# Optimization experiments

Hardware: AMD Instinct MI355X
Metric: run time of the kernel (lower is better)

Reference implementation:

```python
import jax, jax.numpy as jnp
import numpy as np

N_NODES = 100000
N_EDGES = 1600000
D = 128


def sage_conv(x, src, dst, W_l, W_r, b):
    # mean aggregation of source-node features at destination nodes
    msgs = x[src]  # [E, D] gather
    agg = jax.ops.segment_sum(msgs, dst, num_segments=N_NODES)  # [N, D]
    deg = jax.ops.segment_sum(jnp.ones((src.shape[0],), x.dtype), dst,
                              num_segments=N_NODES)
    agg = agg / jnp.maximum(deg, 1.0)[:, None]
    # PyG SAGEConv: lin_l(agg) + lin_r(x) (bias lives in lin_l)
    return agg @ W_l + x @ W_r + b


def setup_inputs() -> dict:
    key = jax.random.key(0)
    ks = jax.random.split(key, 8)
    s = 1.0 / np.sqrt(D)
    x = jax.random.normal(ks[0], (N_NODES, D), dtype=jnp.float32)
    edge_index = jax.random.randint(ks[1], (2, N_EDGES), 0, N_NODES, dtype=jnp.int64)
    W_l1 = jax.random.normal(ks[2], (D, D), dtype=jnp.float32) * s
    W_r1 = jax.random.normal(ks[3], (D, D), dtype=jnp.float32) * s
    b1 = jnp.zeros((D,), dtype=jnp.float32)
    W_l2 = jax.random.normal(ks[4], (D, D), dtype=jnp.float32) * s
    W_r2 = jax.random.normal(ks[5], (D, D), dtype=jnp.float32) * s
    b2 = jnp.zeros((D,), dtype=jnp.float32)
    return {"x": x, "edge_index": edge_index, "W_l1": W_l1, "W_r1": W_r1,
            "b1": b1, "W_l2": W_l2, "W_r2": W_r2, "b2": b2}


def reference(x, edge_index, W_l1, W_r1, b1, W_l2, W_r2, b2):
    src, dst = edge_index[0], edge_index[1]
    h = jax.nn.relu(sage_conv(x, src, dst, W_l1, W_r1, b1))
    h = jax.nn.relu(sage_conv(h, src, dst, W_l2, W_r2, b2))
    return h
```

## Files before the change

kernel.cpp:

```cpp
#include <hip/hip_runtime.h>
#include <hip/hip_bf16.h>
#include <stdint.h>

#define D 128
#define BCAP 18432
typedef unsigned short u16;
typedef unsigned int u32;
typedef __attribute__((ext_vector_type(8))) short bf16x8;
typedef __attribute__((ext_vector_type(4))) float f32x4;
typedef __attribute__((ext_vector_type(2))) float f32x2;
typedef __attribute__((ext_vector_type(2))) unsigned int u32x2;

__device__ inline float bf16lo_to_f(u32 v) {
    u32 u = v << 16; return __builtin_bit_cast(float, u);
}
__device__ inline float bf16hi_to_f(u32 v) {
    u32 u = v & 0xFFFF0000u; return __builtin_bit_cast(float, u);
}
__device__ inline u16 f_to_bf16(float f) {
    u32 u = __builtin_bit_cast(u32, f);
    u += 0x7FFFu + ((u >> 16) & 1u);
    return (u16)(u >> 16);
}
__device__ inline u32 pack_bf16(float a, float b) {
    return (u32)f_to_bf16(a) | ((u32)f_to_bf16(b) << 16);
}

__global__ void zero_ints(int* __restrict__ p, int n) {
    int i = blockIdx.x * blockDim.x + threadIdx.x;
    if (i < n) p[i] = 0;
}

__global__ __launch_bounds__(256) void prep_fused(
    const int* __restrict__ src, const int* __restrict__ dst, int E, int nbuck, int binB,
    uint2* __restrict__ pairs, int* __restrict__ bcur,
    const float* __restrict__ x, u16* __restrict__ xb, int nf4, int convB,
    const float* __restrict__ Wl1, const float* __restrict__ Wr1,
    const float* __restrict__ Wl2, const float* __restrict__ Wr2,
    u16* __restrict__ WT1, u16* __restrict__ WT2) {
    __shared__ int hist[128], gb[128], loc[128];
    int tid = threadIdx.x;
    int bid = blockIdx.x;
    if (bid < binB) {
        if (tid < 128) { hist[tid] = 0; loc[tid] = 0; }
        __syncthreads();
        int base = bid * 4096;
        int d[16], b[16];
        #pragma unroll
        for (int i = 0; i < 16; ++i) {
            int e = base + i * 256 + tid;
            d[i] = (e < E) ? dst[e] : -1;
            b[i] = (d[i] >= 0) ? (d[i] >> 10) : -1;
            if (b[i] >= 0) atomicAdd(&hist[b[i]], 1);
        }
        __syncthreads();
        if (tid < nbuck && hist[tid] > 0) gb[tid] = atomicAdd(&bcur[tid], hist[tid]);
        __syncthreads();
        #pragma unroll
        for (int i = 0; i < 16; ++i) {
            if (b[i] >= 0) {
                int e = base + i * 256 + tid;
                int s = src[e];
                int r = atomicAdd(&loc[b[i]], 1);
                int pos = gb[b[i]] + r;
                if (pos < BCAP)
                    pairs[(size_t)b[i] * BCAP + pos] = make_uint2((u32)s, (u32)d[i]);
            }
        }
    } else if (bid < binB + convB) {
        int idx = (bid - binB) * 256 + tid;
        int stride = convB * 256;
        const float4* xf = (const float4*)x;
        uint2* xo = (uint2*)xb;
        for (int i = idx; i < nf4; i += stride) {
            float4 v = xf[i];
            xo[i] = make_uint2(pack_bf16(v.x, v.y), pack_bf16(v.z, v.w));
        }
    } else {
        int id = (bid - binB - convB) * 256 + tid;
        if (id < 2 * 128 * 256) {
            int which = id >> 15;
            int rem = id & 32767;
            int n = rem >> 8;
            int k = rem & 255;
            const float* Wl = which ? Wl2 : Wl1;
            const float* Wr = which ? Wr2 : Wr1;
            float v = (k < 128) ? Wl[k * 128 + n] : Wr[(k - 128) * 128 + n];
            u16* WT = which ? WT2 : WT1;
            WT[n * 256 + k] = f_to_bf16(v);
        }
    }
}

__global__ __launch_bounds__(256) void build_csr(
    const uint2* __restrict__ pairs, const int* __restrict__ bcur, int N,
    int* __restrict__ cnt, int* __restrict__ seg_start, int* __restrict__ gtotal,
    int* __restrict__ csr_src) {
    __shared__ int cnt_l[1024];
    __shared__ int off_l[1024];
    __shared__ int sblk[256];
    __shared__ int gbase_s;
    int tid = threadIdx.x;
    int bk = blockIdx.x;
    int n0 = bk << 10;
    int nN = min(1024, N - n0);
    #pragma unroll
    for (int i = 0; i < 4; ++i) cnt_l[tid * 4 + i] = 0;
    __syncthreads();
    int m = min(bcur[bk], BCAP);
    const uint2* P = pairs + (size_t)bk * BCAP;
    for (int i = tid; i < m; i += 256) {
        uint2 p = P[i];
        atomicAdd(&cnt_l[(int)p.y - n0], 1);
    }
    __syncthreads();
    int c0 = cnt_l[tid * 4], c1 = cnt_l[tid * 4 + 1], c2 = cnt_l[tid * 4 + 2], c3 = cnt_l[tid * 4 + 3];
    int mysum = c0 + c1 + c2 + c3;
    sblk[tid] = mysum;
    for (int off = 1; off < 256; off <<= 1) {
        __syncthreads();
        int u = (tid >= off) ? sblk[tid - off] : 0;
        __syncthreads();
        sblk[tid] += u;
    }
    int excl = sblk[tid] - mysum;
    off_l[tid * 4]     = excl;
    off_l[tid * 4 + 1] = excl + c0;
    off_l[tid * 4 + 2] = excl + c0 + c1;
    off_l[tid * 4 + 3] = excl + c0 + c1 + c2;
    if (tid == 255) gbase_s = atomicAdd(gtotal, sblk[255]);
    __syncthreads();
    int gbase = gbase_s;
    #pragma unroll
    for (int i = 0; i < 4; ++i) {
        int j = tid * 4 + i;
        if (j < nN) {
            cnt[n0 + j] = cnt_l[j];
            seg_start[n0 + j] = gbase + off_l[j];
        }
    }
    __syncthreads();
    #pragma unroll
    for (int i = 0; i < 4; ++i) cnt_l[tid * 4 + i] = 0;
    __syncthreads();
    for (int i = tid; i < m; i += 256) {
        uint2 p = P[i];
        int dl = (int)p.y - n0;
        int r = atomicAdd(&cnt_l[dl], 1);
        csr_src[gbase + off_l[dl] + r] = (int)p.x;
    }
}

__global__ __launch_bounds__(256) void aggregate_bf16(
    const u16* __restrict__ xb, const int* __restrict__ csr_src,
    const int* __restrict__ seg_start, const int* __restrict__ cnt,
    int N, u16* __restrict__ agg) {
    int wave = threadIdx.x >> 6;
    int lane = threadIdx.x & 63;
    int n = blockIdx.x * (blockDim.x >> 6) + wave;
    if (n >= N) return;
    int s0 = seg_start[n];
    int deg = cnt[n];
    int sub = lane & 15;
    int eoff = lane >> 4;

    f32x2 acc2[4];
    #pragma unroll
    for (int i = 0; i < 4; ++i) acc2[i] = (f32x2){0.f, 0.f};

    for (int c0 = 0; c0 < deg; c0 += 64) {
        int chunkN = min(deg - c0, 64);
        int myidx = (lane < chunkN) ? csr_src[s0 + c0 + lane] : 0;
        for (int e0 = 0; e0 < chunkN; e0 += 16) {
            uint4 v[4];
            bool act[4];
            #pragma unroll
            for (int j = 0; j < 4; ++j) {
                int ej = e0 + j * 4 + eoff;
                act[j] = (ej < chunkN);
                if (e0 + j * 4 < chunkN) {
                    int es = act[j] ? ej : (chunkN - 1);
                    int s = __shfl(myidx, es & 63);
                    v[j] = ((const uint4*)(xb + (size_t)s * 128))[sub];
                }
            }
            #pragma unroll
            for (int j = 0; j < 4; ++j) {
                if (act[j]) {
                    u32 w;
                    w = v[j].x; acc2[0] += __builtin_bit_cast(f32x2, (u32x2){w << 16, w & 0xFFFF0000u});
                    w = v[j].y; acc2[1] += __builtin_bit_cast(f32x2, (u32x2){w << 16, w & 0xFFFF0000u});
                    w = v[j].z; acc2[2] += __builtin_bit_cast(f32x2, (u32x2){w << 16, w & 0xFFFF0000u});
                    w = v[j].w; acc2[3] += __builtin_bit_cast(f32x2, (u32x2){w << 16, w & 0xFFFF0000u});
                }
            }
        }
    }

    float a[8];
    #pragma unroll
    for (int i = 0; i < 4; ++i) { a[2 * i] = acc2[i].x; a[2 * i + 1] = acc2[i].y; }
    #pragma unroll
    for (int i = 0; i < 8; ++i) {
        a[i] += __shfl_xor(a[i], 16);
        a[i] += __shfl_xor(a[i], 32);
    }

    if (eoff == 0) {
        float inv = 1.0f / fmaxf((float)deg, 1.0f);
        uint4 o;
        o.x = pack_bf16(a[0] * inv, a[1] * inv);
        o.y = pack_bf16(a[2] * inv, a[3] * inv);
        o.z = pack_bf16(a[4] * inv, a[5] * inv);
        o.w = pack_bf16(a[6] * inv, a[7] * inv);
        ((uint4*)(agg + (size_t)n * 128))[sub] = o;
    }
}

template<int OUT_BF16>
__global__ __launch_bounds__(256) void sage_gemm(
    const u16* __restrict__ Aa, const u16* __restrict__ Ax,
    const u16* __restrict__ WT, const float* __restrict__ bias,
    void* __restrict__ out, int N) {
    __shared__ u16 Bl[128 * 256];
    int tid = threadIdx.x;

    {
        const uint4* Wg = (const uint4*)WT;
        uint4* Bl4 = (uint4*)Bl;
        #pragma unroll
        for (int i = 0; i < 16; ++i) {
            int cid = tid + 256 * i;
            int n = cid >> 5;
            int kc = cid & 31;
            Bl4[(n << 5) | (kc ^ (n & 15))] = Wg[cid];
        }
    }
    __syncthreads();

    int wavein = tid >> 6;
    int lane = tid & 63;
    int col = lane & 15;
    int chunk = lane >> 4;
    int wid = blockIdx.x * 4 + wavein;

    size_t m0 = (size_t)wid * 32 + col;
    size_t m1 = m0 + 16;
    size_t m0c = (m0 < (size_t)N) ? m0 : (size_t)(N - 1);
    size_t m1c = (m1 < (size_t)N) ? m1 : (size_t)(N - 1);

    const bf16x8* a0p = (const bf16x8*)(Aa + m0c * 128 + chunk * 8);
    const bf16x8* a1p = (const bf16x8*)(Aa + m1c * 128 + chunk * 8);
    const bf16x8* x0p = (const bf16x8*)(Ax + m0c * 128 + chunk * 8);
    const bf16x8* x1p = (const bf16x8*)(Ax + m1c * 128 + chunk * 8);

    f32x4 acc0[8], acc1[8];
    #pragma unroll
    for (int t = 0; t < 8; ++t) {
        acc0[t] = (f32x4){0.f, 0.f, 0.f, 0.f};
        acc1[t] = (f32x4){0.f, 0.f, 0.f, 0.f};
    }

    #pragma unroll
    for (int s = 0; s < 4; ++s) {
        bf16x8 a0 = a0p[s * 4];
        bf16x8 a1 = a1p[s * 4];
        int kc = s * 4 + chunk;
        #pragma unroll
        for (int t = 0; t < 8; ++t) {
            const bf16x8* bp = (const bf16x8*)(Bl + (((16 * t + col) << 8) | ((kc ^ col) << 3)));
            bf16x8 b = *bp;
            acc0[t] = __builtin_amdgcn_mfma_f32_16x16x32_bf16(a0, b, acc0[t], 0, 0, 0);
            acc1[t] = __builtin_amdgcn_mfma_f32_16x16x32_bf16(a1, b, acc1[t], 0, 0, 0);
        }
    }
    #pragma unroll
    for (int s = 0; s < 4; ++s) {
        bf16x8 a0 = x0p[s * 4];
        bf16x8 a1 = x1p[s * 4];
        int kc = 16 + s * 4 + chunk;
        #pragma unroll
        for (int t = 0; t < 8; ++t) {
            const bf16x8* bp = (const bf16x8*)(Bl + (((16 * t + col) << 8) | ((kc ^ col) << 3)));
            bf16x8 b = *bp;
            acc0[t] = __builtin_amdgcn_mfma_f32_16x16x32_bf16(a0, b, acc0[t], 0, 0, 0);
            acc1[t] = __builtin_amdgcn_mfma_f32_16x16x32_bf16(a1, b, acc1[t], 0, 0, 0);
        }
    }

    #pragma unroll
    for (int mt = 0; mt < 2; ++mt) {
        size_t row0 = (size_t)wid * 32 + mt * 16 + chunk * 4;
        #pragma unroll
        for (int t = 0; t < 8; ++t) {
            int n = 16 * t + col;
            float bv = bias[n];
            f32x4 a = mt ? acc1[t] : acc0[t];
            #pragma unroll
            for (int r = 0; r < 4; ++r) {
                size_t row = row0 + r;
                if (row < (size_t)N) {
                    float v = fmaxf(a[r] + bv, 0.f);
                    if (OUT_BF16) ((u16*)out)[row * 128 + n] = f_to_bf16(v);
                    else          ((float*)out)[row * 128 + n] = v;
                }
            }
        }
    }
}

extern "C" void kernel_launch(void* const* d_in, const int* in_sizes, int n_in,
                              void* d_out, int out_size, void* d_ws, size_t ws_size,
                              hipStream_t stream) {
    const float* x   = (const float*)d_in[0];
    const int*   ei  = (const int*)d_in[1];
    const float* Wl1 = (const float*)d_in[2];
    const float* Wr1 = (const float*)d_in[3];
    const float* b1  = (const float*)d_in[4];
    const float* Wl2 = (const float*)d_in[5];
    const float* Wr2 = (const float*)d_in[6];
    const float* b2  = (const float*)d_in[7];
    float* out       = (float*)d_out;

    int N = in_sizes[0] / D;
    int E = in_sizes[1] / 2;
    const int* src = ei;
    const int* dst = ei + E;
    int nbuck = (N + 1023) >> 10;

    char* ws = (char*)d_ws;
    int* cnt       = (int*)ws;  ws += (size_t)N * 4;
    int* seg_start = (int*)ws;  ws += (size_t)N * 4;
    int* bcur      = (int*)ws;  ws += 128 * 4;
    int* gtotal    = (int*)ws;  ws += 4 * 4;
    ws = (char*)(((uintptr_t)ws + 255) & ~(uintptr_t)255);
    int* csr_src   = (int*)ws;  ws += (size_t)E * 4;
    ws = (char*)(((uintptr_t)ws + 255) & ~(uintptr_t)255);
    u16* WT1       = (u16*)ws;  ws += (size_t)128 * 256 * 2;
    u16* WT2       = (u16*)ws;  ws += (size_t)128 * 256 * 2;
    ws = (char*)(((uintptr_t)ws + 255) & ~(uintptr_t)255);
    u16* aggb      = (u16*)ws;  ws += (size_t)N * 128 * 2;
    ws = (char*)(((uintptr_t)ws + 255) & ~(uintptr_t)255);
    u16* h1b       = (u16*)ws;  ws += (size_t)N * 128 * 2;
    u16* xb        = (u16*)d_out;
    uint2* pairs   = (uint2*)aggb;

    zero_ints<<<1, 256, 0, stream>>>(bcur, 132);

    int binB  = (E + 4095) / 4096;
    int convB = 2048;
    int nf4   = N * (D / 4);
    prep_fused<<<binB + convB + 256, 256, 0, stream>>>(
        src, dst, E, nbuck, binB, pairs, bcur,
        x, xb, nf4, convB, Wl1, Wr1, Wl2, Wr2, WT1, WT2);

    build_csr<<<nbuck, 256, 0, stream>>>(pairs, bcur, N, cnt, seg_start, gtotal, csr_src);

    int aggBlocks = (N + 3) / 4;
    int gemmBlocks = (N + 127) / 128;

    aggregate_bf16<<<aggBlocks, 256, 0, stream>>>(xb, csr_src, seg_start, cnt, N, aggb);
    sage_gemm<1><<<gemmBlocks, 256, 0, stream>>>(aggb, xb, WT1, b1, h1b, N);

    aggregate_bf16<<<aggBlocks, 256, 0, stream>>>(h1b, csr_src, seg_start, cnt, N, aggb);
    sage_gemm<0><<<gemmBlocks, 256, 0, stream>>>(aggb, h1b, WT2, b2, out, N);
}
```

Before: 344.8 us.

## Pad bucket counters, widen build_csr to 1024 threads, skip inactive gather loads

Bucket cursors are spaced 32 ints apart so blocks doing atomics on different buckets no longer contend on the same cache line. build_csr now runs 1024 threads per block, one per node slot, which simplifies the scan and doubles pair-scan parallelism but lengthens the scan to 10 barrier-separated steps. The aggregate kernel no longer issues redundant loads for inactive tail edges; instead it predicates the load. These are small, mostly independent tweaks to the preprocessing and gather stages.

```diff
diff --git a/kernel.cpp b/kernel.cpp
--- a/kernel.cpp
+++ b/kernel.cpp
@@ -4,6 +4,7 @@
 
 #define D 128
 #define BCAP 18432
+#define CPAD 32
 typedef unsigned short u16;
 typedef unsigned int u32;
 typedef __attribute__((ext_vector_type(8))) short bf16x8;
@@ -11,12 +12,6 @@
 typedef __attribute__((ext_vector_type(2))) float f32x2;
 typedef __attribute__((ext_vector_type(2))) unsigned int u32x2;
 
-__device__ inline float bf16lo_to_f(u32 v) {
-    u32 u = v << 16; return __builtin_bit_cast(float, u);
-}
-__device__ inline float bf16hi_to_f(u32 v) {
-    u32 u = v & 0xFFFF0000u; return __builtin_bit_cast(float, u);
-}
 __device__ inline u16 f_to_bf16(float f) {
     u32 u = __builtin_bit_cast(u32, f);
     u += 0x7FFFu + ((u >> 16) & 1u);
@@ -54,7 +49,7 @@
             if (b[i] >= 0) atomicAdd(&hist[b[i]], 1);
         }
         __syncthreads();
-        if (tid < nbuck && hist[tid] > 0) gb[tid] = atomicAdd(&bcur[tid], hist[tid]);
+        if (tid < nbuck && hist[tid] > 0) gb[tid] = atomicAdd(&bcur[tid * CPAD], hist[tid]);
         __syncthreads();
         #pragma unroll
         for (int i = 0; i < 16; ++i) {
@@ -92,58 +87,47 @@
     }
 }
 
-__global__ __launch_bounds__(256) void build_csr(
+__global__ __launch_bounds__(1024) void build_csr(
     const uint2* __restrict__ pairs, const int* __restrict__ bcur, int N,
     int* __restrict__ cnt, int* __restrict__ seg_start, int* __restrict__ gtotal,
     int* __restrict__ csr_src) {
     __shared__ int cnt_l[1024];
     __shared__ int off_l[1024];
-    __shared__ int sblk[256];
+    __shared__ int sblk[1024];
     __shared__ int gbase_s;
     int tid = threadIdx.x;
     int bk = blockIdx.x;
     int n0 = bk << 10;
     int nN = min(1024, N - n0);
-    #pragma unroll
-    for (int i = 0; i < 4; ++i) cnt_l[tid * 4 + i] = 0;
-    __syncthreads();
-    int m = min(bcur[bk], BCAP);
+    cnt_l[tid] = 0;
+    __syncthreads();
+    int m = min(bcur[bk * CPAD], BCAP);
     const uint2* P = pairs + (size_t)bk * BCAP;
-    for (int i = tid; i < m; i += 256) {
+    for (int i = tid; i < m; i += 1024) {
         uint2 p = P[i];
         atomicAdd(&cnt_l[(int)p.y - n0], 1);
     }
     __syncthreads();
-    int c0 = cnt_l[tid * 4], c1 = cnt_l[tid * 4 + 1], c2 = cnt_l[tid * 4 + 2], c3 = cnt_l[tid * 4 + 3];
-    int mysum = c0 + c1 + c2 + c3;
-    sblk[tid] = mysum;
-    for (int off = 1; off < 256; off <<= 1) {
+    int c = cnt_l[tid];
+    sblk[tid] = c;
+    for (int off = 1; off < 1024; off <<= 1) {
         __syncthreads();
         int u = (tid >= off) ? sblk[tid - off] : 0;
         __syncthreads();
         sblk[tid] += u;
     }
-    int excl = sblk[tid] - mysum;
-    off_l[tid * 4]     = excl;
-    off_l[tid * 4 + 1] = excl + c0;
-    off_l[tid * 4 + 2] = excl + c0 + c1;
-    off_l[tid * 4 + 3] = excl + c0 + c1 + c2;
-    if (tid == 255) gbase_s = atomicAdd(gtotal, sblk[255]);
+    int excl = sblk[tid] - c;
+    off_l[tid] = excl;
+    if (tid == 1023) gbase_s = atomicAdd(gtotal, sblk[1023]);
     __syncthreads();
     int gbase = gbase_s;
-    #pragma unroll
-    for (int i = 0; i < 4; ++i) {
-        int j = tid * 4 + i;
-        if (j < nN) {
-            cnt[n0 + j] = cnt_l[j];
-            seg_start[n0 + j] = gbase + off_l[j];
-        }
-    }
-    __syncthreads();
-    #pragma unroll
-    for (int i = 0; i < 4; ++i) cnt_l[tid * 4 + i] = 0;
-    __syncthreads();
-    for (int i = tid; i < m; i += 256) {
+    if (tid < nN) {
+        cnt[n0 + tid] = c;
+        seg_start[n0 + tid] = gbase + excl;
+    }
+    cnt_l[tid] = 0;
+    __syncthreads();
+    for (int i = tid; i < m; i += 1024) {
         uint2 p = P[i];
         int dl = (int)p.y - n0;
         int r = atomicAdd(&cnt_l[dl], 1);
@@ -173,20 +157,19 @@
         int myidx = (lane < chunkN) ? csr_src[s0 + c0 + lane] : 0;
         for (int e0 = 0; e0 < chunkN; e0 += 16) {
             uint4 v[4];
-            bool act[4];
             #pragma unroll
             for (int j = 0; j < 4; ++j) {
                 int ej = e0 + j * 4 + eoff;
-                act[j] = (ej < chunkN);
                 if (e0 + j * 4 < chunkN) {
-                    int es = act[j] ? ej : (chunkN - 1);
-                    int s = __shfl(myidx, es & 63);
-                    v[j] = ((const uint4*)(xb + (size_t)s * 128))[sub];
+                    int s = __shfl(myidx, ej & 63);
+                    if (ej < chunkN)
+                        v[j] = ((const uint4*)(xb + (size_t)s * 128))[sub];
                 }
             }
             #pragma unroll
             for (int j = 0; j < 4; ++j) {
-                if (act[j]) {
+                int ej = e0 + j * 4 + eoff;
+                if (ej < chunkN) {
                     u32 w;
                     w = v[j].x; acc2[0] += __builtin_bit_cast(f32x2, (u32x2){w << 16, w & 0xFFFF0000u});
                     w = v[j].y; acc2[1] += __builtin_bit_cast(f32x2, (u32x2){w << 16, w & 0xFFFF0000u});
@@ -331,7 +314,7 @@
     char* ws = (char*)d_ws;
     int* cnt       = (int*)ws;  ws += (size_t)N * 4;
     int* seg_start = (int*)ws;  ws += (size_t)N * 4;
-    int* bcur      = (int*)ws;  ws += 128 * 4;
+    int* bcur      = (int*)ws;  ws += 128 * CPAD * 4;
     int* gtotal    = (int*)ws;  ws += 4 * 4;
     ws = (char*)(((uintptr_t)ws + 255) & ~(uintptr_t)255);
     int* csr_src   = (int*)ws;  ws += (size_t)E * 4;
@@ -345,7 +328,7 @@
     u16* xb        = (u16*)d_out;
     uint2* pairs   = (uint2*)aggb;
 
-    zero_ints<<<1, 256, 0, stream>>>(bcur, 132);
+    zero_ints<<<(128 * CPAD + 4 + 255) / 256, 256, 0, stream>>>(bcur, 128 * CPAD + 4);
 
     int binB  = (E + 4095) / 4096;
     int convB = 2048;
@@ -354,7 +337,7 @@
         src, dst, E, nbuck, binB, pairs, bcur,
         x, xb, nf4, convB, Wl1, Wr1, Wl2, Wr2, WT1, WT2);
 
-    build_csr<<<nbuck, 256, 0, stream>>>(pairs, bcur, N, cnt, seg_start, gtotal, csr_src);
+    build_csr<<<nbuck, 1024, 0, stream>>>(pairs, bcur, N, cnt, seg_start, gtotal, csr_src);
 
     int aggBlocks = (N + 3) / 4;
     int gemmBlocks = (N + 127) / 128;
```

Result: faster. 327.5 us (-5.0%).
